# Kernel tuning notes

Measured on AMD Instinct MI355X. Metric: run time of the kernel, lower is better.

Reference implementation:

```python
import jax, jax.numpy as jnp
import numpy as np

N = 8192
D = 256


def setup_inputs() -> dict:
    key = jax.random.key(0)
    ks = jax.random.split(key, 10)
    s = 1.0 / np.sqrt(D)
    inp = {
        "embeddings": jax.random.normal(ks[0], (N, D), dtype=jnp.float32),
        "adjacency": jax.random.randint(ks[1], (N, N), 0, 2, dtype=jnp.int32),
        "Wq": jax.random.uniform(ks[2], (D, D), jnp.float32, -s, s),
        "bq": jax.random.uniform(ks[3], (D,), jnp.float32, -s, s),
        "Wk": jax.random.uniform(ks[4], (D, D), jnp.float32, -s, s),
        "bk": jax.random.uniform(ks[5], (D,), jnp.float32, -s, s),
        "Wv": jax.random.uniform(ks[6], (D, D), jnp.float32, -s, s),
        "bv": jax.random.uniform(ks[7], (D,), jnp.float32, -s, s),
        "Wo": jax.random.uniform(ks[8], (D, D), jnp.float32, -s, s),
        "bo": jax.random.uniform(ks[9], (D,), jnp.float32, -s, s),
    }
    return inp


def reference(embeddings, adjacency, Wq, bq, Wk, bk, Wv, bv, Wo, bo):
    # Q/K/V projections (torch Linear: x @ W.T + b)
    Q = embeddings @ Wq.T + bq            # [N, D]
    K = embeddings @ Wk.T + bk            # [N, D]
    V = embeddings @ Wv.T + bv            # [N, D]
    scale = 1.0 / jnp.sqrt(jnp.asarray(D, dtype=embeddings.dtype))
    scores = (Q @ K.T) * scale            # [N, N]
    scores = jnp.where(adjacency == 0, jnp.asarray(-1e9, scores.dtype), scores)
    attn = jax.nn.softmax(scores, axis=-1)  # dropout is identity in eval mode
    context = attn @ V                    # [N, D]
    return context @ Wo.T + bo
```

## Files before the change

kernel.cpp:

```cpp
#include <hip/hip_runtime.h>
#include <hip/hip_bf16.h>


#define LOG2E 1.44269504088896340736f
#define MASKVAL -3.0e38f
#define MINIT   -1.0e38f

using f32x4 = __attribute__((ext_vector_type(4))) float;
using s16x8 = __attribute__((ext_vector_type(8))) short;
using s16x4 = __attribute__((ext_vector_type(4))) short;

__device__ __forceinline__ void gl_lds16(void* l, const void* g) {
  __builtin_amdgcn_global_load_lds(
      (const __attribute__((address_space(1))) void*)g,
      (__attribute__((address_space(3))) void*)l, 16, 0, 0);
}

__device__ __forceinline__ short f2bf(float x) {
  union { float f; unsigned u; } v; v.f = x;
  unsigned r = v.u + 0x7fffu + ((v.u >> 16) & 1u);
  return (short)(r >> 16);
}

__device__ __forceinline__ s16x8 cvt_frag(f32x4 a, f32x4 b) {
  s16x8 r;
  r[0]=f2bf(a[0]); r[1]=f2bf(a[1]); r[2]=f2bf(a[2]); r[3]=f2bf(a[3]);
  r[4]=f2bf(b[0]); r[5]=f2bf(b[1]); r[6]=f2bf(b[2]); r[7]=f2bf(b[3]);
  return r;
}

__device__ __forceinline__ f32x4 mfma16(s16x8 a, s16x8 b, f32x4 c) {
  return __builtin_amdgcn_mfma_f32_16x16x32_bf16(a, b, c, 0, 0, 0);
}

template<bool A_BF16, bool OUT_BF16, bool TRANS_OUT>
__global__ __launch_bounds__(256, 4)
void proj_kernel(const void* __restrict__ Ap, const float* __restrict__ W,
                 const float* __restrict__ bias, void* __restrict__ outp,
                 float scale)
{
  __shared__ __align__(16) char ldsA[A_BF16 ? 8192 : 16384];
  __shared__ __align__(16) char ldsB[16384];
  const int tid = threadIdx.x;
  const int lane = tid & 63, w = tid >> 6;
  const int wr = w >> 1, wc = w & 1;
  const int l15 = lane & 15, lhi = lane >> 4;
  const int m0 = blockIdx.x * 64, n0 = blockIdx.y * 64;
  const char* Ab = (const char*)Ap;
  const char* Wb = (const char*)W;

  f32x4 acc[2][2] = {};

  for (int k0 = 0; k0 < 256; k0 += 64) {
    if (A_BF16) {
#pragma unroll
      for (int i = 0; i < 2; ++i) {
        int o = tid * 16 + i * 4096;
        int row = o >> 7, inrow = o & 127;
        gl_lds16(ldsA + o, Ab + (size_t)(m0 + row) * 512 + k0 * 2 + (inrow ^ ((row & 7) << 4)));
      }
    } else {
#pragma unroll
      for (int i = 0; i < 4; ++i) {
        int o = tid * 16 + i * 4096;
        int row = o >> 8, inrow = o & 255;
        gl_lds16(ldsA + o, Ab + (size_t)(m0 + row) * 1024 + k0 * 4 + (inrow ^ ((row & 7) << 4)));
      }
    }
#pragma unroll
    for (int i = 0; i < 4; ++i) {
      int o = tid * 16 + i * 4096;
      int row = o >> 8, inrow = o & 255;
      gl_lds16(ldsB + o, Wb + (size_t)(n0 + row) * 1024 + k0 * 4 + (inrow ^ ((row & 7) << 4)));
    }
    __syncthreads();

#pragma unroll
    for (int ks = 0; ks < 2; ++ks) {
      s16x8 af[2], bfr[2];
#pragma unroll
      for (int m = 0; m < 2; ++m) {
        int row = wr * 32 + m * 16 + l15;
        if (A_BF16) {
          int c = ks * 64 + lhi * 16;
          af[m] = *(const s16x8*)(ldsA + row * 128 + (c ^ ((row & 7) << 4)));
        } else {
          int c = ks * 128 + lhi * 32;
          f32x4 lo = *(const f32x4*)(ldsA + row * 256 + (c ^ ((row & 7) << 4)));
          f32x4 hi = *(const f32x4*)(ldsA + row * 256 + ((c + 16) ^ ((row & 7) << 4)));
          af[m] = cvt_frag(lo, hi);
        }
      }
#pragma unroll
      for (int n = 0; n < 2; ++n) {
        int row = wc * 32 + n * 16 + l15;
        int c = ks * 128 + lhi * 32;
        f32x4 lo = *(const f32x4*)(ldsB + row * 256 + (c ^ ((row & 7) << 4)));
        f32x4 hi = *(const f32x4*)(ldsB + row * 256 + ((c + 16) ^ ((row & 7) << 4)));
        bfr[n] = cvt_frag(lo, hi);
      }
#pragma unroll
      for (int m = 0; m < 2; ++m)
#pragma unroll
        for (int n = 0; n < 2; ++n)
          acc[m][n] = mfma16(af[m], bfr[n], acc[m][n]);
    }
    __syncthreads();
  }

#pragma unroll
  for (int n = 0; n < 2; ++n) {
    int col = n0 + wc * 32 + n * 16 + l15;
    float bv = bias[col];
#pragma unroll
    for (int m = 0; m < 2; ++m) {
      int rbase = m0 + wr * 32 + m * 16 + lhi * 4;
      if (TRANS_OUT) {
        s16x4 pk;
#pragma unroll
        for (int r = 0; r < 4; ++r) pk[r] = f2bf((acc[m][n][r] + bv) * scale);
        *(s16x4*)((unsigned short*)outp + (size_t)col * 8192 + rbase) = pk;
      } else if (OUT_BF16) {
#pragma unroll
        for (int r = 0; r < 4; ++r)
          ((unsigned short*)outp)[(size_t)(rbase + r) * 256 + col] =
              (unsigned short)f2bf((acc[m][n][r] + bv) * scale);
      } else {
#pragma unroll
        for (int r = 0; r < 4; ++r)
          ((float*)outp)[(size_t)(rbase + r) * 256 + col] = (acc[m][n][r] + bv) * scale;
      }
    }
  }
}

template<int SPLIT, bool DIRECT, bool PACC_BF16>
__global__ __launch_bounds__(256, 2)
void attn_kernel(const unsigned short* __restrict__ Qb, const char* __restrict__ Kb,
                 const char* __restrict__ VbT, const int* __restrict__ adj,
                 void* __restrict__ pacc, float* __restrict__ pm,
                 float* __restrict__ pl, unsigned short* __restrict__ CX)
{
  __shared__ __align__(16) char ldsK[32768];
  __shared__ __align__(16) char ldsV[32768];
  __shared__ __align__(16) char ldsP[16384];
  const int tid = threadIdx.x, lane = tid & 63, w = tid >> 6;
  const int l15 = lane & 15, lhi = lane >> 4;
  const int qt = blockIdx.x / SPLIT, sp = blockIdx.x % SPLIT;
  const int q0 = qt * 128 + w * 32;
  char* myP = ldsP + w * 4096;
  const int kv_begin = sp * (8192 / SPLIT);
  const int NT = 8192 / SPLIT / 64;

  s16x8 qf[2][8];
#pragma unroll
  for (int f = 0; f < 2; ++f) {
    const unsigned short* qp = Qb + (size_t)(q0 + f * 16 + l15) * 256 + lhi * 8;
#pragma unroll
    for (int ks = 0; ks < 8; ++ks) qf[f][ks] = *(const s16x8*)(qp + ks * 32);
  }

  f32x4 ctx[2][16] = {};
  float m_run[2][4], l_run[2][4];
#pragma unroll
  for (int f = 0; f < 2; ++f)
#pragma unroll
    for (int r = 0; r < 4; ++r) { m_run[f][r] = MINIT; l_run[f][r] = 0.f; }

  for (int t = 0; t < NT; ++t) {
    const int kv0 = kv_begin + t * 64;

    {
      const char* kg = Kb + (size_t)kv0 * 512;
#pragma unroll
      for (int i = 0; i < 8; ++i) {
        int o = tid * 16 + i * 4096;
        int row = o >> 9, inrow = o & 511;
        gl_lds16(ldsK + o, kg + row * 512 + (inrow ^ ((row & 7) << 4)));
      }
#pragma unroll
      for (int i = 0; i < 8; ++i) {
        int o = tid * 16 + i * 4096;
        int row = o >> 7, inrow = o & 127;
        gl_lds16(ldsV + o, VbT + (size_t)row * 16384 + (size_t)kv0 * 2 + (inrow ^ ((row & 7) << 4)));
      }
    }

    int am[2][4][4];
#pragma unroll
    for (int f = 0; f < 2; ++f) {
      const int* ap = adj + (size_t)(q0 + f * 16 + lhi * 4) * 8192 + kv0 + l15;
#pragma unroll
      for (int r = 0; r < 4; ++r)
#pragma unroll
        for (int cg = 0; cg < 4; ++cg)
          am[f][r][cg] = ap[(size_t)r * 8192 + cg * 16];
    }

    __syncthreads();

    f32x4 sacc[2][4] = {};
    __builtin_amdgcn_s_setprio(1);
#pragma unroll
    for (int ks = 0; ks < 8; ++ks)
#pragma unroll
      for (int cg = 0; cg < 4; ++cg) {
        int row = cg * 16 + l15;
        s16x8 kf = *(const s16x8*)(ldsK + row * 512 + ((ks * 64 + lhi * 16) ^ ((row & 7) << 4)));
        sacc[0][cg] = mfma16(qf[0][ks], kf, sacc[0][cg]);
        sacc[1][cg] = mfma16(qf[1][ks], kf, sacc[1][cg]);
      }
    __builtin_amdgcn_s_setprio(0);

#pragma unroll
    for (int f = 0; f < 2; ++f)
#pragma unroll
      for (int r = 0; r < 4; ++r)
#pragma unroll
        for (int cg = 0; cg < 4; ++cg)
          if (am[f][r][cg] == 0) sacc[f][cg][r] = MASKVAL;

    float tmax[2][4];
#pragma unroll
    for (int f = 0; f < 2; ++f)
#pragma unroll
      for (int r = 0; r < 4; ++r)
        tmax[f][r] = fmaxf(fmaxf(sacc[f][0][r], sacc[f][1][r]),
                           fmaxf(sacc[f][2][r], sacc[f][3][r]));
#pragma unroll
    for (int mk = 1; mk <= 8; mk <<= 1)
#pragma unroll
      for (int f = 0; f < 2; ++f)
#pragma unroll
        for (int r = 0; r < 4; ++r)
          tmax[f][r] = fmaxf(tmax[f][r], __shfl_xor(tmax[f][r], mk, 64));

    float need = MASKVAL;
#pragma unroll
    for (int f = 0; f < 2; ++f)
#pragma unroll
      for (int r = 0; r < 4; ++r)
        need = fmaxf(need, tmax[f][r] - m_run[f][r]);
    if (!__all(need <= 8.0f)) {
#pragma unroll
      for (int f = 0; f < 2; ++f) {
        f32x4 fv;
#pragma unroll
        for (int r = 0; r < 4; ++r) {
          float mnew = fmaxf(m_run[f][r], tmax[f][r]);
          float fs = __builtin_amdgcn_exp2f((m_run[f][r] - mnew) * LOG2E);
          m_run[f][r] = mnew; l_run[f][r] *= fs; fv[r] = fs;
        }
#pragma unroll
        for (int dm = 0; dm < 16; ++dm) ctx[f][dm] *= fv;
      }
    }

#pragma unroll
    for (int f = 0; f < 2; ++f)
#pragma unroll
      for (int cg = 0; cg < 4; ++cg)
#pragma unroll
        for (int r = 0; r < 4; ++r) {
          float p = __builtin_amdgcn_exp2f((sacc[f][cg][r] - m_run[f][r]) * LOG2E);
          l_run[f][r] += p;
          int row = f * 16 + lhi * 4 + r;
          int cb = (cg * 16 + l15) * 2;
          *(short*)(myP + row * 128 + (cb ^ ((row & 7) << 4))) = f2bf(p);
        }

    __builtin_amdgcn_s_setprio(1);
#pragma unroll
    for (int ks = 0; ks < 2; ++ks) {
      s16x8 pf[2];
#pragma unroll
      for (int f = 0; f < 2; ++f) {
        int prow = f * 16 + l15;
        pf[f] = *(const s16x8*)(myP + prow * 128 + (((ks * 32 + lhi * 8) * 2) ^ ((prow & 7) << 4)));
      }
#pragma unroll
      for (int dm = 0; dm < 16; ++dm) {
        int vrow = dm * 16 + l15;
        s16x8 vf = *(const s16x8*)(ldsV + vrow * 128 + (((ks * 32 + lhi * 8) * 2) ^ ((vrow & 7) << 4)));
        ctx[0][dm] = mfma16(pf[0], vf, ctx[0][dm]);
        ctx[1][dm] = mfma16(pf[1], vf, ctx[1][dm]);
      }
    }
    __builtin_amdgcn_s_setprio(0);
    __syncthreads();
  }

#pragma unroll
  for (int mk = 1; mk <= 8; mk <<= 1)
#pragma unroll
    for (int f = 0; f < 2; ++f)
#pragma unroll
      for (int r = 0; r < 4; ++r)
        l_run[f][r] += __shfl_xor(l_run[f][r], mk, 64);

  if (DIRECT) {
#pragma unroll
    for (int f = 0; f < 2; ++f)
#pragma unroll
      for (int r = 0; r < 4; ++r) {
        float inv = 1.0f / l_run[f][r];
        size_t rowb = (size_t)(q0 + f * 16 + lhi * 4 + r) * 256 + l15;
#pragma unroll
        for (int dm = 0; dm < 16; ++dm)
          CX[rowb + dm * 16] = (unsigned short)f2bf(ctx[f][dm][r] * inv);
      }
  } else {
#pragma unroll
    for (int f = 0; f < 2; ++f)
#pragma unroll
      for (int r = 0; r < 4; ++r) {
        size_t rowb = (size_t)sp * 8192 * 256 +
                      (size_t)(q0 + f * 16 + lhi * 4 + r) * 256 + l15;
        if (PACC_BF16) {
#pragma unroll
          for (int dm = 0; dm < 16; ++dm)
            ((unsigned short*)pacc)[rowb + dm * 16] = (unsigned short)f2bf(ctx[f][dm][r]);
        } else {
#pragma unroll
          for (int dm = 0; dm < 16; ++dm)
            ((float*)pacc)[rowb + dm * 16] = ctx[f][dm][r];
        }
      }
    if (l15 == 0) {
#pragma unroll
      for (int f = 0; f < 2; ++f)
#pragma unroll
        for (int r = 0; r < 4; ++r) {
          pm[(size_t)sp * 8192 + q0 + f * 16 + lhi * 4 + r] = m_run[f][r];
          pl[(size_t)sp * 8192 + q0 + f * 16 + lhi * 4 + r] = l_run[f][r];
        }
    }
  }
}

template<bool PACC_BF16>
__global__ __launch_bounds__(256)
void combine_kernel(const void* __restrict__ pacc, const float* __restrict__ pm,
                    const float* __restrict__ pl, unsigned short* __restrict__ cx)
{
  const int row = blockIdx.x;
  const int d = threadIdx.x;
  float M = MINIT;
#pragma unroll
  for (int s = 0; s < 8; ++s) M = fmaxf(M, pm[s * 8192 + row]);
  float L = 0.f, v = 0.f;
#pragma unroll
  for (int s = 0; s < 8; ++s) {
    float ws = __builtin_amdgcn_exp2f((pm[s * 8192 + row] - M) * LOG2E);
    L += ws * pl[s * 8192 + row];
    size_t idx = (size_t)s * 8192 * 256 + (size_t)row * 256 + d;
    float pv;
    if (PACC_BF16) {
      union { unsigned u; float f; } c; c.u = (unsigned)((const unsigned short*)pacc)[idx] << 16;
      pv = c.f;
    } else {
      pv = ((const float*)pacc)[idx];
    }
    v += ws * pv;
  }
  cx[(size_t)row * 256 + d] = (unsigned short)f2bf(v / L);
}

extern "C" void kernel_launch(void* const* d_in, const int* in_sizes, int n_in,
                              void* d_out, int out_size, void* d_ws, size_t ws_size,
                              hipStream_t stream)
{
  const float* E  = (const float*)d_in[0];
  const int*  adj = (const int*)d_in[1];
  const float* Wq = (const float*)d_in[2];
  const float* bq = (const float*)d_in[3];
  const float* Wk = (const float*)d_in[4];
  const float* bk = (const float*)d_in[5];
  const float* Wv = (const float*)d_in[6];
  const float* bv = (const float*)d_in[7];
  const float* Wo = (const float*)d_in[8];
  const float* bo = (const float*)d_in[9];

  char* ws = (char*)d_ws;
  unsigned short* Qb = (unsigned short*)(ws);
  unsigned short* Kb = (unsigned short*)(ws + ((size_t)4 << 20));
  unsigned short* VT = (unsigned short*)(ws + ((size_t)8 << 20));
  unsigned short* CX = (unsigned short*)(ws + ((size_t)12 << 20));
  char* pacc = ws + ((size_t)16 << 20);

  dim3 g(128, 4), b(256);
  hipLaunchKernelGGL((proj_kernel<false, true, false>), g, b, 0, stream, E, Wq, bq, Qb, 0.0625f);
  hipLaunchKernelGGL((proj_kernel<false, true, false>), g, b, 0, stream, E, Wk, bk, Kb, 1.0f);
  hipLaunchKernelGGL((proj_kernel<false, true, true>),  g, b, 0, stream, E, Wv, bv, VT, 1.0f);

  const size_t PACC_F32_BYTES  = (size_t)8 * 8192 * 256 * 4;
  const size_t PACC_BF16_BYTES = (size_t)8 * 8192 * 256 * 2;
  const size_t PMPL = (size_t)8 * 8192 * 4;
  const size_t NEED_F32  = ((size_t)16 << 20) + PACC_F32_BYTES + 2 * PMPL;
  const size_t NEED_BF16 = ((size_t)16 << 20) + PACC_BF16_BYTES + 2 * PMPL;

  if (ws_size >= NEED_F32) {
    float* pm = (float*)(pacc + PACC_F32_BYTES);
    float* pl = pm + 8 * 8192;
    hipLaunchKernelGGL((attn_kernel<8, false, false>), dim3(512), b, 0, stream,
                       Qb, (const char*)Kb, (const char*)VT, adj, pacc, pm, pl, CX);
    hipLaunchKernelGGL((combine_kernel<false>), dim3(8192), b, 0, stream, pacc, pm, pl, CX);
  } else if (ws_size >= NEED_BF16) {
    float* pm = (float*)(pacc + PACC_BF16_BYTES);
    float* pl = pm + 8 * 8192;
    hipLaunchKernelGGL((attn_kernel<8, false, true>), dim3(512), b, 0, stream,
                       Qb, (const char*)Kb, (const char*)VT, adj, pacc, pm, pl, CX);
    hipLaunchKernelGGL((combine_kernel<true>), dim3(8192), b, 0, stream, pacc, pm, pl, CX);
  } else {
    float* pm = (float*)pacc; float* pl = pm + 8192;
    hipLaunchKernelGGL((attn_kernel<1, true, false>), dim3(64), b, 0, stream,
                       Qb, (const char*)Kb, (const char*)VT, adj, pacc, pm, pl, CX);
  }
  hipLaunchKernelGGL((proj_kernel<true, false, false>), g, b, 0, stream, CX, Wo, bo, d_out, 1.0f);
}
```

Before: 675.8 us.

## Fuse QKV projections, double-buffer attention KV tiles, ballot-pack adjacency mask

Replaces the three LDS-staged projection launches with one fused QKV kernel that loads fragments straight from global memory into registers. The Wo projection is rewritten the same way. The attention kernel moves to 512-thread blocks covering 256 queries with 32-wide KV tiles, double-buffered in LDS so the next tile loads while the current one computes. Adjacency is now read with coalesced row-contiguous loads and turned into bitmasks via wave ballots. This aims to cut launch overhead, redundant embedding reads, uncoalesced mask loads and load stalls, at the cost of more register pressure and smaller MFMA tiles per iteration.

Result: faster. 618.5 us (-8.5%).

```diff
diff --git a/kernel.cpp b/kernel.cpp
--- a/kernel.cpp
+++ b/kernel.cpp
@@ -33,124 +33,134 @@
   return __builtin_amdgcn_mfma_f32_16x16x32_bf16(a, b, c, 0, 0, 0);
 }
 
-template<bool A_BF16, bool OUT_BF16, bool TRANS_OUT>
-__global__ __launch_bounds__(256, 4)
-void proj_kernel(const void* __restrict__ Ap, const float* __restrict__ W,
-                 const float* __restrict__ bias, void* __restrict__ outp,
-                 float scale)
+__global__ __launch_bounds__(256, 2)
+void qkv_kernel(const float* __restrict__ E,
+                const float* __restrict__ Wq, const float* __restrict__ bq,
+                const float* __restrict__ Wk, const float* __restrict__ bk,
+                const float* __restrict__ Wv, const float* __restrict__ bv,
+                unsigned short* __restrict__ Qb, unsigned short* __restrict__ Kb,
+                unsigned short* __restrict__ VT)
 {
-  __shared__ __align__(16) char ldsA[A_BF16 ? 8192 : 16384];
-  __shared__ __align__(16) char ldsB[16384];
-  const int tid = threadIdx.x;
-  const int lane = tid & 63, w = tid >> 6;
+  const int tid = threadIdx.x, lane = tid & 63, w = tid >> 6;
   const int wr = w >> 1, wc = w & 1;
   const int l15 = lane & 15, lhi = lane >> 4;
-  const int m0 = blockIdx.x * 64, n0 = blockIdx.y * 64;
-  const char* Ab = (const char*)Ap;
-  const char* Wb = (const char*)W;
+  const int m0 = blockIdx.x * 64 + wr * 32;
+  const int n0 = blockIdx.y * 64 + wc * 32;
+
+  s16x8 af[2][8];
+#pragma unroll
+  for (int m = 0; m < 2; ++m) {
+    const float* ap = E + (size_t)(m0 + m * 16 + l15) * 256 + lhi * 8;
+#pragma unroll
+    for (int ks = 0; ks < 8; ++ks) {
+      f32x4 lo = *(const f32x4*)(ap + ks * 32);
+      f32x4 hi = *(const f32x4*)(ap + ks * 32 + 4);
+      af[m][ks] = cvt_frag(lo, hi);
+    }
+  }
+
+  const float* Ws[3] = {Wq, Wk, Wv};
+  f32x4 acc[3][2][2] = {};
+#pragma unroll
+  for (int mtx = 0; mtx < 3; ++mtx)
+#pragma unroll
+    for (int n = 0; n < 2; ++n) {
+      const float* bp = Ws[mtx] + (size_t)(n0 + n * 16 + l15) * 256 + lhi * 8;
+#pragma unroll
+      for (int ks = 0; ks < 8; ++ks) {
+        f32x4 lo = *(const f32x4*)(bp + ks * 32);
+        f32x4 hi = *(const f32x4*)(bp + ks * 32 + 4);
+        s16x8 bf = cvt_frag(lo, hi);
+#pragma unroll
+        for (int m = 0; m < 2; ++m)
+          acc[mtx][m][n] = mfma16(af[m][ks], bf, acc[mtx][m][n]);
+      }
+    }
+
+#pragma unroll
+  for (int n = 0; n < 2; ++n) {
+    int col = n0 + n * 16 + l15;
+    float bvq = bq[col], bvk = bk[col], bvv = bv[col];
+#pragma unroll
+    for (int m = 0; m < 2; ++m) {
+      int rbase = m0 + m * 16 + lhi * 4;
+#pragma unroll
+      for (int r = 0; r < 4; ++r) {
+        Qb[(size_t)(rbase + r) * 256 + col] = (unsigned short)f2bf((acc[0][m][n][r] + bvq) * 0.0625f);
+        Kb[(size_t)(rbase + r) * 256 + col] = (unsigned short)f2bf(acc[1][m][n][r] + bvk);
+      }
+      s16x4 pk;
+#pragma unroll
+      for (int r = 0; r < 4; ++r) pk[r] = f2bf(acc[2][m][n][r] + bvv);
+      *(s16x4*)(VT + (size_t)col * 8192 + rbase) = pk;
+    }
+  }
+}
+
+__global__ __launch_bounds__(256, 2)
+void projo_kernel(const unsigned short* __restrict__ CX, const float* __restrict__ Wo,
+                  const float* __restrict__ bo, float* __restrict__ outp)
+{
+  const int tid = threadIdx.x, lane = tid & 63, w = tid >> 6;
+  const int wr = w >> 1, wc = w & 1;
+  const int l15 = lane & 15, lhi = lane >> 4;
+  const int m0 = blockIdx.x * 64 + wr * 32;
+  const int n0 = blockIdx.y * 64 + wc * 32;
+
+  s16x8 af[2][8];
+#pragma unroll
+  for (int m = 0; m < 2; ++m) {
+    const unsigned short* ap = CX + (size_t)(m0 + m * 16 + l15) * 256 + lhi * 8;
+#pragma unroll
+    for (int ks = 0; ks < 8; ++ks) af[m][ks] = *(const s16x8*)(ap + ks * 32);
+  }
 
   f32x4 acc[2][2] = {};
-
-  for (int k0 = 0; k0 < 256; k0 += 64) {
-    if (A_BF16) {
-#pragma unroll
-      for (int i = 0; i < 2; ++i) {
-        int o = tid * 16 + i * 4096;
-        int row = o >> 7, inrow = o & 127;
-        gl_lds16(ldsA + o, Ab + (size_t)(m0 + row) * 512 + k0 * 2 + (inrow ^ ((row & 7) << 4)));
-      }
-    } else {
-#pragma unroll
-      for (int i = 0; i < 4; ++i) {
-        int o = tid * 16 + i * 4096;
-        int row = o >> 8, inrow = o & 255;
-        gl_lds16(ldsA + o, Ab + (size_t)(m0 + row) * 1024 + k0 * 4 + (inrow ^ ((row & 7) << 4)));
-      }
-    }
-#pragma unroll
-    for (int i = 0; i < 4; ++i) {
-      int o = tid * 16 + i * 4096;
-      int row = o >> 8, inrow = o & 255;
-      gl_lds16(ldsB + o, Wb + (size_t)(n0 + row) * 1024 + k0 * 4 + (inrow ^ ((row & 7) << 4)));
-    }
-    __syncthreads();
-
-#pragma unroll
-    for (int ks = 0; ks < 2; ++ks) {
-      s16x8 af[2], bfr[2];
-#pragma unroll
-      for (int m = 0; m < 2; ++m) {
-        int row = wr * 32 + m * 16 + l15;
-        if (A_BF16) {
-          int c = ks * 64 + lhi * 16;
-          af[m] = *(const s16x8*)(ldsA + row * 128 + (c ^ ((row & 7) << 4)));
-        } else {
-          int c = ks * 128 + lhi * 32;
-          f32x4 lo = *(const f32x4*)(ldsA + row * 256 + (c ^ ((row & 7) << 4)));
-          f32x4 hi = *(const f32x4*)(ldsA + row * 256 + ((c + 16) ^ ((row & 7) << 4)));
-          af[m] = cvt_frag(lo, hi);
-        }
-      }
-#pragma unroll
-      for (int n = 0; n < 2; ++n) {
-        int row = wc * 32 + n * 16 + l15;
-        int c = ks * 128 + lhi * 32;
-        f32x4 lo = *(const f32x4*)(ldsB + row * 256 + (c ^ ((row & 7) << 4)));
-        f32x4 hi = *(const f32x4*)(ldsB + row * 256 + ((c + 16) ^ ((row & 7) << 4)));
-        bfr[n] = cvt_frag(lo, hi);
-      }
+#pragma unroll
+  for (int n = 0; n < 2; ++n) {
+    const float* bp = Wo + (size_t)(n0 + n * 16 + l15) * 256 + lhi * 8;
+#pragma unroll
+    for (int ks = 0; ks < 8; ++ks) {
+      f32x4 lo = *(const f32x4*)(bp + ks * 32);
+      f32x4 hi = *(const f32x4*)(bp + ks * 32 + 4);
+      s16x8 bf = cvt_frag(lo, hi);
 #pragma unroll
       for (int m = 0; m < 2; ++m)
-#pragma unroll
-        for (int n = 0; n < 2; ++n)
-          acc[m][n] = mfma16(af[m], bfr[n], acc[m][n]);
-    }
-    __syncthreads();
+        acc[m][n] = mfma16(af[m][ks], bf, acc[m][n]);
+    }
   }
 
 #pragma unroll
   for (int n = 0; n < 2; ++n) {
-    int col = n0 + wc * 32 + n * 16 + l15;
-    float bv = bias[col];
+    int col = n0 + n * 16 + l15;
+    float bv = bo[col];
 #pragma unroll
     for (int m = 0; m < 2; ++m) {
-      int rbase = m0 + wr * 32 + m * 16 + lhi * 4;
-      if (TRANS_OUT) {
-        s16x4 pk;
-#pragma unroll
-        for (int r = 0; r < 4; ++r) pk[r] = f2bf((acc[m][n][r] + bv) * scale);
-        *(s16x4*)((unsigned short*)outp + (size_t)col * 8192 + rbase) = pk;
-      } else if (OUT_BF16) {
-#pragma unroll
-        for (int r = 0; r < 4; ++r)
-          ((unsigned short*)outp)[(size_t)(rbase + r) * 256 + col] =
-              (unsigned short)f2bf((acc[m][n][r] + bv) * scale);
-      } else {
-#pragma unroll
-        for (int r = 0; r < 4; ++r)
-          ((float*)outp)[(size_t)(rbase + r) * 256 + col] = (acc[m][n][r] + bv) * scale;
-      }
+      int rbase = m0 + m * 16 + lhi * 4;
+#pragma unroll
+      for (int r = 0; r < 4; ++r)
+        outp[(size_t)(rbase + r) * 256 + col] = acc[m][n][r] + bv;
     }
   }
 }
 
 template<int SPLIT, bool DIRECT, bool PACC_BF16>
-__global__ __launch_bounds__(256, 2)
+__global__ __launch_bounds__(512, 2)
 void attn_kernel(const unsigned short* __restrict__ Qb, const char* __restrict__ Kb,
                  const char* __restrict__ VbT, const int* __restrict__ adj,
                  void* __restrict__ pacc, float* __restrict__ pm,
                  float* __restrict__ pl, unsigned short* __restrict__ CX)
 {
-  __shared__ __align__(16) char ldsK[32768];
-  __shared__ __align__(16) char ldsV[32768];
-  __shared__ __align__(16) char ldsP[16384];
+  __shared__ __align__(16) char ldsK[2][16384];
+  __shared__ __align__(16) char ldsV[2][16384];
+  __shared__ __align__(16) char ldsP[8][2048];
   const int tid = threadIdx.x, lane = tid & 63, w = tid >> 6;
   const int l15 = lane & 15, lhi = lane >> 4;
   const int qt = blockIdx.x / SPLIT, sp = blockIdx.x % SPLIT;
-  const int q0 = qt * 128 + w * 32;
-  char* myP = ldsP + w * 4096;
+  const int q0 = qt * 256 + w * 32;
+  char* myP = ldsP[w];
   const int kv_begin = sp * (8192 / SPLIT);
-  const int NT = 8192 / SPLIT / 64;
+  const int NT = 8192 / SPLIT / 32;
 
   s16x8 qf[2][8];
 #pragma unroll
@@ -167,66 +177,80 @@
 #pragma unroll
     for (int r = 0; r < 4; ++r) { m_run[f][r] = MINIT; l_run[f][r] = 0.f; }
 
+  auto STAGE = [&](int buf, int tt) {
+    const int kv0 = kv_begin + tt * 32;
+    const char* kg = Kb + (size_t)kv0 * 512;
+#pragma unroll
+    for (int i = 0; i < 2; ++i) {
+      int o = tid * 16 + i * 8192;
+      int row = o >> 9, inrow = o & 511;
+      gl_lds16(&ldsK[buf][o], kg + row * 512 + (inrow ^ ((row & 7) << 4)));
+    }
+#pragma unroll
+    for (int i = 0; i < 2; ++i) {
+      int o = tid * 16 + i * 8192;
+      int row = o >> 6, inrow = o & 63;
+      gl_lds16(&ldsV[buf][o], VbT + (size_t)row * 16384 + (size_t)kv0 * 2 + (inrow ^ ((row & 3) << 4)));
+    }
+  };
+
+  STAGE(0, 0);
+  __syncthreads();
+
+  const int* abase = adj + (size_t)(q0 + (lane >> 5)) * 8192 + (lane & 31);
+
   for (int t = 0; t < NT; ++t) {
-    const int kv0 = kv_begin + t * 64;
-
+    const int cur = t & 1;
+    const int kv0 = kv_begin + t * 32;
+
+    int av[16];
     {
-      const char* kg = Kb + (size_t)kv0 * 512;
-#pragma unroll
-      for (int i = 0; i < 8; ++i) {
-        int o = tid * 16 + i * 4096;
-        int row = o >> 9, inrow = o & 511;
-        gl_lds16(ldsK + o, kg + row * 512 + (inrow ^ ((row & 7) << 4)));
-      }
-#pragma unroll
-      for (int i = 0; i < 8; ++i) {
-        int o = tid * 16 + i * 4096;
-        int row = o >> 7, inrow = o & 127;
-        gl_lds16(ldsV + o, VbT + (size_t)row * 16384 + (size_t)kv0 * 2 + (inrow ^ ((row & 7) << 4)));
-      }
-    }
-
-    int am[2][4][4];
-#pragma unroll
-    for (int f = 0; f < 2; ++f) {
-      const int* ap = adj + (size_t)(q0 + f * 16 + lhi * 4) * 8192 + kv0 + l15;
-#pragma unroll
-      for (int r = 0; r < 4; ++r)
-#pragma unroll
-        for (int cg = 0; cg < 4; ++cg)
-          am[f][r][cg] = ap[(size_t)r * 8192 + cg * 16];
-    }
-
-    __syncthreads();
-
-    f32x4 sacc[2][4] = {};
+      const int* ap = abase + kv0;
+#pragma unroll
+      for (int j = 0; j < 16; ++j) av[j] = ap[(size_t)j * 2 * 8192];
+    }
+    if (t + 1 < NT) STAGE(cur ^ 1, t + 1);
+
+    f32x4 sacc[2][2] = {};
     __builtin_amdgcn_s_setprio(1);
 #pragma unroll
     for (int ks = 0; ks < 8; ++ks)
 #pragma unroll
-      for (int cg = 0; cg < 4; ++cg) {
+      for (int cg = 0; cg < 2; ++cg) {
         int row = cg * 16 + l15;
-        s16x8 kf = *(const s16x8*)(ldsK + row * 512 + ((ks * 64 + lhi * 16) ^ ((row & 7) << 4)));
+        s16x8 kf = *(const s16x8*)(&ldsK[cur][row * 512 + ((ks * 64 + lhi * 16) ^ ((row & 7) << 4))]);
         sacc[0][cg] = mfma16(qf[0][ks], kf, sacc[0][cg]);
         sacc[1][cg] = mfma16(qf[1][ks], kf, sacc[1][cg]);
       }
     __builtin_amdgcn_s_setprio(0);
 
+    unsigned bmv[2][4] = {};
+#pragma unroll
+    for (int j = 0; j < 16; ++j) {
+      unsigned long long b = __ballot(av[j] != 0);
+      unsigned lo = (unsigned)b, hi = (unsigned)(b >> 32);
+      const int row0 = 2 * j;
+      const int f = row0 >> 4, g = (row0 >> 2) & 3, r = row0 & 3;
+      bmv[f][r]     = (lhi == g) ? lo : bmv[f][r];
+      bmv[f][r + 1] = (lhi == g) ? hi : bmv[f][r + 1];
+    }
+
+#pragma unroll
+    for (int f = 0; f < 2; ++f)
+#pragma unroll
+      for (int r = 0; r < 4; ++r) {
+        unsigned ms = bmv[f][r] >> l15;
+#pragma unroll
+        for (int cg = 0; cg < 2; ++cg)
+          if (!((ms >> (cg * 16)) & 1u)) sacc[f][cg][r] = MASKVAL;
+      }
+
+    float tmax[2][4];
 #pragma unroll
     for (int f = 0; f < 2; ++f)
 #pragma unroll
       for (int r = 0; r < 4; ++r)
-#pragma unroll
-        for (int cg = 0; cg < 4; ++cg)
-          if (am[f][r][cg] == 0) sacc[f][cg][r] = MASKVAL;
-
-    float tmax[2][4];
-#pragma unroll
-    for (int f = 0; f < 2; ++f)
-#pragma unroll
-      for (int r = 0; r < 4; ++r)
-        tmax[f][r] = fmaxf(fmaxf(sacc[f][0][r], sacc[f][1][r]),
-                           fmaxf(sacc[f][2][r], sacc[f][3][r]));
+        tmax[f][r] = fmaxf(sacc[f][0][r], sacc[f][1][r]);
 #pragma unroll
     for (int mk = 1; mk <= 8; mk <<= 1)
 #pragma unroll
@@ -259,34 +283,32 @@
 #pragma unroll
     for (int f = 0; f < 2; ++f)
 #pragma unroll
-      for (int cg = 0; cg < 4; ++cg)
+      for (int cg = 0; cg < 2; ++cg)
 #pragma unroll
         for (int r = 0; r < 4; ++r) {
           float p = __builtin_amdgcn_exp2f((sacc[f][cg][r] - m_run[f][r]) * LOG2E);
           l_run[f][r] += p;
           int row = f * 16 + lhi * 4 + r;
           int cb = (cg * 16 + l15) * 2;
-          *(short*)(myP + row * 128 + (cb ^ ((row & 7) << 4))) = f2bf(p);
+          *(short*)(myP + row * 64 + (cb ^ ((row & 3) << 4))) = f2bf(p);
         }
 
     __builtin_amdgcn_s_setprio(1);
-#pragma unroll
-    for (int ks = 0; ks < 2; ++ks) {
-      s16x8 pf[2];
-#pragma unroll
-      for (int f = 0; f < 2; ++f) {
-        int prow = f * 16 + l15;
-        pf[f] = *(const s16x8*)(myP + prow * 128 + (((ks * 32 + lhi * 8) * 2) ^ ((prow & 7) << 4)));
-      }
-#pragma unroll
-      for (int dm = 0; dm < 16; ++dm) {
-        int vrow = dm * 16 + l15;
-        s16x8 vf = *(const s16x8*)(ldsV + vrow * 128 + (((ks * 32 + lhi * 8) * 2) ^ ((vrow & 7) << 4)));
-        ctx[0][dm] = mfma16(pf[0], vf, ctx[0][dm]);
-        ctx[1][dm] = mfma16(pf[1], vf, ctx[1][dm]);
-      }
+    s16x8 pf[2];
+#pragma unroll
+    for (int f = 0; f < 2; ++f) {
+      int prow = f * 16 + l15;
+      pf[f] = *(const s16x8*)(myP + prow * 64 + ((lhi * 16) ^ ((prow & 3) << 4)));
+    }
+#pragma unroll
+    for (int dm = 0; dm < 16; ++dm) {
+      int vrow = dm * 16 + l15;
+      s16x8 vf = *(const s16x8*)(&ldsV[cur][vrow * 64 + ((lhi * 16) ^ ((vrow & 3) << 4))]);
+      ctx[0][dm] = mfma16(pf[0], vf, ctx[0][dm]);
+      ctx[1][dm] = mfma16(pf[1], vf, ctx[1][dm]);
     }
     __builtin_amdgcn_s_setprio(0);
+
     __syncthreads();
   }
 
@@ -388,10 +410,8 @@
   unsigned short* CX = (unsigned short*)(ws + ((size_t)12 << 20));
   char* pacc = ws + ((size_t)16 << 20);
 
-  dim3 g(128, 4), b(256);
-  hipLaunchKernelGGL((proj_kernel<false, true, false>), g, b, 0, stream, E, Wq, bq, Qb, 0.0625f);
-  hipLaunchKernelGGL((proj_kernel<false, true, false>), g, b, 0, stream, E, Wk, bk, Kb, 1.0f);
-  hipLaunchKernelGGL((proj_kernel<false, true, true>),  g, b, 0, stream, E, Wv, bv, VT, 1.0f);
+  hipLaunchKernelGGL(qkv_kernel, dim3(128, 4), dim3(256), 0, stream,
+                     E, Wq, bq, Wk, bk, Wv, bv, Qb, Kb, VT);
 
   const size_t PACC_F32_BYTES  = (size_t)8 * 8192 * 256 * 4;
   const size_t PACC_BF16_BYTES = (size_t)8 * 8192 * 256 * 2;
@@ -402,19 +422,19 @@
   if (ws_size >= NEED_F32) {
     float* pm = (float*)(pacc + PACC_F32_BYTES);
     float* pl = pm + 8 * 8192;
-    hipLaunchKernelGGL((attn_kernel<8, false, false>), dim3(512), b, 0, stream,
+    hipLaunchKernelGGL((attn_kernel<8, false, false>), dim3(256), dim3(512), 0, stream,
                        Qb, (const char*)Kb, (const char*)VT, adj, pacc, pm, pl, CX);
-    hipLaunchKernelGGL((combine_kernel<false>), dim3(8192), b, 0, stream, pacc, pm, pl, CX);
+    hipLaunchKernelGGL((combine_kernel<false>), dim3(8192), dim3(256), 0, stream, pacc, pm, pl, CX);
   } else if (ws_size >= NEED_BF16) {
     float* pm = (float*)(pacc + PACC_BF16_BYTES);
     float* pl = pm + 8 * 8192;
-    hipLaunchKernelGGL((attn_kernel<8, false, true>), dim3(512), b, 0, stream,
+    hipLaunchKernelGGL((attn_kernel<8, false, true>), dim3(256), dim3(512), 0, stream,
                        Qb, (const char*)Kb, (const char*)VT, adj, pacc, pm, pl, CX);
-    hipLaunchKernelGGL((combine_kernel<true>), dim3(8192), b, 0, stream, pacc, pm, pl, CX);
+    hipLaunchKernelGGL((combine_kernel<true>), dim3(8192), dim3(256), 0, stream, pacc, pm, pl, CX);
   } else {
     float* pm = (float*)pacc; float* pl = pm + 8192;
-    hipLaunchKernelGGL((attn_kernel<1, true, false>), dim3(64), b, 0, stream,
+    hipLaunchKernelGGL((attn_kernel<1, true, false>), dim3(32), dim3(512), 0, stream,
                        Qb, (const char*)Kb, (const char*)VT, adj, pacc, pm, pl, CX);
   }
-  hipLaunchKernelGGL((proj_kernel<true, false, false>), g, b, 0, stream, CX, Wo, bo, d_out, 1.0f);
-}
+  hipLaunchKernelGGL(projo_kernel, dim3(128, 4), dim3(256), 0, stream, CX, Wo, bo, (float*)d_out);
+}
```
